# Optimization experiments

Hardware: AMD Instinct MI355X
Metric: run time of the kernel (lower is better)

## Reference

```python
import jax, jax.numpy as jnp
import numpy as np

B = 16384   # tokens
K = 2       # top_k
E = 64      # num_experts
H = 512     # hidden_dim
F = 1024    # expert ffn dim


def setup_inputs() -> dict:
    key = jax.random.key(0)
    k1, k2, k3, k4, k5 = jax.random.split(key, 5)
    hidden_states = jax.random.normal(k1, (B, H), dtype=jnp.float32)
    expert_weights = jax.nn.softmax(jax.random.normal(k2, (B, K), dtype=jnp.float32), axis=-1)
    # Balanced routing: exactly B*K/E assignments per expert (random permutation
    # of a tiled pattern). This is a valid routing for the module and lets the
    # reference use a fixed-capacity grouped GEMM with zero token dropping.
    flat_ids = jax.random.permutation(k3, jnp.tile(jnp.arange(E, dtype=jnp.int32), (B * K) // E))
    expert_ids = flat_ids.reshape(B, K)
    W1 = jax.random.normal(k4, (E, H, F), dtype=jnp.float32) * (1.0 / np.sqrt(H))
    W2 = jax.random.normal(k5, (E, F, H), dtype=jnp.float32) * (1.0 / np.sqrt(F))
    return {"hidden_states": hidden_states, "expert_weights": expert_weights,
            "expert_ids": expert_ids, "W1": W1, "W2": W2}


def reference(hidden_states, expert_weights, expert_ids, W1, W2):
    # Faithful to ExpertGrouping.group_dispatch: every (token, slot) assignment
    # is run through its expert, scaled by its routing weight, and index_add'ed
    # back into the per-token output. Since assignments within an expert are
    # order-independent, we sort assignments by expert id and run one grouped
    # batched GEMM (the fused equivalent of the per-group/per-expert loops).
    b, h = hidden_states.shape
    k = expert_ids.shape[1]
    e = W1.shape[0]
    n = b * k
    cap = n // e  # exact per-expert count (balanced routing)

    flat_ids = expert_ids.reshape(-1)            # [N]
    flat_w = expert_weights.reshape(-1)          # [N]
    token_idx = jnp.arange(n, dtype=jnp.int32) // k  # [N] token for each assignment

    order = jnp.argsort(flat_ids)                # stable sort: groups assignments by expert
    tok_sorted = token_idx[order]                # [N]
    w_sorted = flat_w[order]                     # [N]

    # Gather-dispatch: [E, cap, H]
    xg = hidden_states[tok_sorted].reshape(e, cap, h)
    # Grouped expert FFN (batched over experts)
    hid = jax.nn.silu(jnp.einsum('ech,ehf->ecf', xg, W1))
    yg = jnp.einsum('ecf,efh->ech', hid, W2)     # [E, cap, H]

    # Weighted scatter-combine back to tokens
    weighted = yg.reshape(n, h) * w_sorted[:, None]
    out = jnp.zeros((b, h), dtype=hidden_states.dtype).at[tok_sorted].add(weighted)
    return out
```

## Files before the change

### kernel.cpp

```cpp
#include <hip/hip_runtime.h>
#include <hip/hip_bf16.h>

#define B_TOK 16384
#define TOPK 2
#define NEXP 64
#define HID 512
#define FFN 1024
#define NASSIGN (B_TOK * TOPK)
#define CAP (NASSIGN / NEXP)

typedef unsigned short u16;
typedef __bf16 bf16_t;
typedef bf16_t bf16x8 __attribute__((ext_vector_type(8)));
typedef float f32x4 __attribute__((ext_vector_type(4)));

__device__ __forceinline__ unsigned pkbf(float a, float b) {
  union { bf16_t h[2]; unsigned u; } v;
  v.h[0] = (bf16_t)a; v.h[1] = (bf16_t)b;
  return v.u;
}
__device__ __forceinline__ u16 f2bf(float f) {
  union { bf16_t h; u16 u; } v; v.h = (bf16_t)f; return v.u;
}
__device__ __forceinline__ float bf2f(unsigned u16v) {
  union { unsigned u; float f; } v; v.u = u16v << 16; return v.f;
}

#define GLOAD_LDS16(g, l)                                                     \
  __builtin_amdgcn_global_load_lds((const __attribute__((address_space(1))) void*)(g), \
                                   (__attribute__((address_space(3))) void*)(l), 16, 0, 0)

__global__ void k_route(const int* __restrict__ ids, int* __restrict__ cnt,
                        int* __restrict__ tok_of, int* __restrict__ slot_pos) {
  int n = blockIdx.x * blockDim.x + threadIdx.x;
  if (n >= NASSIGN) return;
  int e = ids[n];
  int r = atomicAdd(&cnt[e], 1);
  int p = e * CAP + r;
  tok_of[p] = n >> 1;
  slot_pos[n] = p;
}

__global__ void k_gather(const float* __restrict__ hs, const int* __restrict__ tok_of,
                         u16* __restrict__ Xg) {
  int p = blockIdx.x * 4 + (threadIdx.x >> 6);
  int lane = threadIdx.x & 63;
  const float4* src = reinterpret_cast<const float4*>(hs + (size_t)tok_of[p] * HID);
  uint2* dst = reinterpret_cast<uint2*>(Xg + (size_t)p * HID);
#pragma unroll
  for (int i = 0; i < 2; i++) {
    float4 v = src[i * 64 + lane];
    uint2 o;
    o.x = pkbf(v.x, v.y);
    o.y = pkbf(v.z, v.w);
    dst[i * 64 + lane] = o;
  }
}

template <int K, int NN, bool SILU>
__global__ __launch_bounds__(256, 2) void k_gemm(const u16* __restrict__ A,
                                                 const float* __restrict__ Wf,
                                                 u16* __restrict__ Cout) {
  constexpr int MT = CAP / 128;
  constexpr int NT = NN / 128;
  constexpr int NWG = NEXP * MT * NT;
  constexpr int Q = NWG / 8;
  constexpr int KT = K / 64;
  int wg = (blockIdx.x % 8) * Q + blockIdx.x / 8;
  int e = wg / (MT * NT);
  int rm = wg % (MT * NT);
  int mt = rm / NT, nt = rm % NT;

  const u16* Ab = A + ((size_t)e * CAP + (size_t)mt * 128) * K;

  __shared__ __align__(16) char smc[65536];

  int t_ = threadIdx.x;
  int lane = t_ & 63, wv = t_ >> 6;
  int wm = wv >> 1, wn = wv & 1;
  int l15 = lane & 15, lhi = lane >> 4;

  int srow = t_ >> 3;
  int gchunk = (t_ & 7) ^ (srow & 7);
  const u16* gA = Ab + (size_t)srow * K + gchunk * 8;
#define STAGE_A(tn)                                                          \
  do {                                                                       \
    char* d_ = smc + ((tn) & 1) * 16384 + wv * 1024;                         \
    const u16* s_ = gA + (size_t)(tn) * 64;                                  \
    GLOAD_LDS16(s_, d_);                                                     \
    GLOAD_LDS16(s_ + (size_t)32 * K, d_ + 4096);                             \
    GLOAD_LDS16(s_ + (size_t)64 * K, d_ + 8192);                             \
    GLOAD_LDS16(s_ + (size_t)96 * K, d_ + 12288);                            \
  } while (0)

  int kunit = t_ >> 5;
  int nunit = t_ & 31;
  const float* gWb = Wf + (size_t)e * K * NN + (size_t)(kunit * 8) * NN +
                     (size_t)nt * 128 + nunit * 4;
  int wbo[4];
#pragma unroll
  for (int i = 0; i < 4; i++) {
    int n = nunit * 4 + i;
    int S = (n ^ (n >> 3)) & 7;
    wbo[i] = 32768 + n * 128 + ((kunit ^ S) << 4);
  }

  f32x4 acc[4][4];
#pragma unroll
  for (int i = 0; i < 4; i++)
#pragma unroll
    for (int j = 0; j < 4; j++) {
      f32x4 z = {0.f, 0.f, 0.f, 0.f};
      acc[i][j] = z;
    }
  bf16x8 a[4][2], b[4][2];

  int aof[4][2], bof[4][2];
#pragma unroll
  for (int f = 0; f < 4; f++) {
    int ar = wm * 64 + f * 16 + l15;
    aof[f][0] = ar * 128 + ((lhi ^ (ar & 7)) << 4);
    aof[f][1] = ar * 128 + (((4 + lhi) ^ (ar & 7)) << 4);
    int br = wn * 64 + f * 16 + l15;
    int Sb = (br ^ (br >> 3)) & 7;
    bof[f][0] = br * 128 + ((lhi ^ Sb) << 4);
    bof[f][1] = br * 128 + (((4 + lhi) ^ Sb) << 4);
  }

#define LOAD_L(tn)                                                           \
  do {                                                                       \
    const float* g_ = gWb + (size_t)(tn) * 64 * NN;                          \
    L0 = *reinterpret_cast<const float4*>(g_);                               \
    L1 = *reinterpret_cast<const float4*>(g_ + (size_t)1 * NN);              \
    L2 = *reinterpret_cast<const float4*>(g_ + (size_t)2 * NN);              \
    L3 = *reinterpret_cast<const float4*>(g_ + (size_t)3 * NN);              \
    L4 = *reinterpret_cast<const float4*>(g_ + (size_t)4 * NN);              \
    L5 = *reinterpret_cast<const float4*>(g_ + (size_t)5 * NN);              \
    L6 = *reinterpret_cast<const float4*>(g_ + (size_t)6 * NN);              \
    L7 = *reinterpret_cast<const float4*>(g_ + (size_t)7 * NN);              \
  } while (0)

#define WRITE_B(bufsel)                                                      \
  do {                                                                       \
    char* w_ = smc + (bufsel) * 16384;                                       \
    _Pragma("unroll") for (int i = 0; i < 4; i++) {                          \
      uint4 v;                                                               \
      v.x = pkbf(L0[i], L1[i]); v.y = pkbf(L2[i], L3[i]);                    \
      v.z = pkbf(L4[i], L5[i]); v.w = pkbf(L6[i], L7[i]);                    \
      *reinterpret_cast<uint4*>(w_ + wbo[i]) = v;                            \
    }                                                                        \
  } while (0)

  float4 L0, L1, L2, L3, L4, L5, L6, L7;

  STAGE_A(0);
  LOAD_L(0);
  asm volatile("s_waitcnt vmcnt(0)" ::: "memory");
  __builtin_amdgcn_sched_barrier(0);
  WRITE_B(0);
  asm volatile("s_waitcnt lgkmcnt(0)" ::: "memory");
  __builtin_amdgcn_sched_barrier(0);
  __builtin_amdgcn_s_barrier();

  for (int t = 0; t < KT; t++) {
    const char* pA = smc + (t & 1) * 16384;
    const char* pB = smc + 32768 + (t & 1) * 16384;
    int nb = (t + 1) & 1;

    if (t + 1 < KT) LOAD_L(t + 1);
#pragma unroll
    for (int f = 0; f < 4; f++) {
      a[f][0] = *reinterpret_cast<const bf16x8*>(pA + aof[f][0]);
      a[f][1] = *reinterpret_cast<const bf16x8*>(pA + aof[f][1]);
      b[f][0] = *reinterpret_cast<const bf16x8*>(pB + bof[f][0]);
      b[f][1] = *reinterpret_cast<const bf16x8*>(pB + bof[f][1]);
    }
    if (t + 1 < KT) STAGE_A(t + 1);
    asm volatile("s_waitcnt lgkmcnt(0)" ::: "memory");
    __builtin_amdgcn_sched_barrier(0);

    __builtin_amdgcn_s_setprio(1);
#pragma unroll
    for (int mf = 0; mf < 4; mf++)
#pragma unroll
      for (int nf = 0; nf < 4; nf++)
#pragma unroll
        for (int kk = 0; kk < 2; kk++)
          acc[mf][nf] = __builtin_amdgcn_mfma_f32_16x16x32_bf16(a[mf][kk], b[nf][kk], acc[mf][nf], 0, 0, 0);
    __builtin_amdgcn_s_setprio(0);

    if (t + 1 < KT) {
      asm volatile("s_waitcnt vmcnt(4)" ::: "memory");
      __builtin_amdgcn_sched_barrier(0);
      WRITE_B(nb);
    }
    asm volatile("s_waitcnt vmcnt(0) lgkmcnt(0)" ::: "memory");
    __builtin_amdgcn_sched_barrier(0);
    __builtin_amdgcn_s_barrier();
  }
#undef STAGE_A
#undef LOAD_L
#undef WRITE_B

#pragma unroll
  for (int mf = 0; mf < 4; mf++) {
#pragma unroll
    for (int nf = 0; nf < 4; nf++) {
#pragma unroll
      for (int rg = 0; rg < 4; rg++) {
        float v = acc[mf][nf][rg];
        int grow = mt * 128 + wm * 64 + mf * 16 + lhi * 4 + rg;
        int gcol = nt * 128 + wn * 64 + nf * 16 + l15;
        size_t off = ((size_t)e * CAP + grow) * NN + gcol;
        if constexpr (SILU) v = v / (1.0f + __expf(-v));
        Cout[off] = f2bf(v);
      }
    }
  }
}

__global__ void k_combine(const u16* __restrict__ yws, const int* __restrict__ slot_pos,
                          const float* __restrict__ w, float* __restrict__ out) {
  int tk = blockIdx.x;
  int t = threadIdx.x;
  int p0 = slot_pos[2 * tk], p1 = slot_pos[2 * tk + 1];
  float w0 = w[2 * tk], w1 = w[2 * tk + 1];
  unsigned ua = reinterpret_cast<const unsigned*>(yws + (size_t)p0 * HID)[t];
  unsigned ub = reinterpret_cast<const unsigned*>(yws + (size_t)p1 * HID)[t];
  float2 o;
  o.x = w0 * bf2f(ua & 0xffffu) + w1 * bf2f(ub & 0xffffu);
  o.y = w0 * bf2f(ua >> 16) + w1 * bf2f(ub >> 16);
  reinterpret_cast<float2*>(out + (size_t)tk * HID)[t] = o;
}

extern "C" void kernel_launch(void* const* d_in, const int* in_sizes, int n_in,
                              void* d_out, int out_size, void* d_ws, size_t ws_size,
                              hipStream_t stream) {
  const float* hs = (const float*)d_in[0];
  const float* wts = (const float*)d_in[1];
  const int* ids = (const int*)d_in[2];
  const float* W1 = (const float*)d_in[3];
  const float* W2 = (const float*)d_in[4];
  float* out = (float*)d_out;

  char* ws = (char*)d_ws;
  size_t o = 0;
  int* cnt = (int*)(ws + o);       o += 1024;
  int* slot_pos = (int*)(ws + o);  o += (size_t)NASSIGN * 4;
  int* tok_of = (int*)(ws + o);    o += (size_t)NASSIGN * 4;
  o = (o + 255) & ~(size_t)255;
  u16* Xg = (u16*)(ws + o);        o += (size_t)NASSIGN * HID * 2;
  u16* hid = (u16*)(ws + o);       o += (size_t)NASSIGN * FFN * 2;
  u16* yws = (u16*)(ws + o);       o += (size_t)NASSIGN * HID * 2;

  hipMemsetAsync(cnt, 0, NEXP * sizeof(int), stream);
  k_route<<<(NASSIGN + 255) / 256, 256, 0, stream>>>(ids, cnt, tok_of, slot_pos);
  k_gather<<<NASSIGN / 4, 256, 0, stream>>>(hs, tok_of, Xg);
  k_gemm<HID, FFN, true><<<NEXP * (CAP / 128) * (FFN / 128), 256, 0, stream>>>(Xg, W1, hid);
  k_gemm<FFN, HID, false><<<NEXP * (CAP / 128) * (HID / 128), 256, 0, stream>>>(hid, W2, yws);
  k_combine<<<B_TOK, 256, 0, stream>>>(yws, slot_pos, wts, out);
}
```

Baseline: 240.5 us.

## Shrink GEMM K-tile to 32 and restructure LDS layout for B operand

Cuts the K step per iteration from 64 to 32, which shrinks LDS use from 64KB to 36KB. The B operand now uses a padded 80-byte row layout instead of an XOR swizzle, loaded as float2 instead of float4. The explicit waitcnt/sched_barrier/setprio scheduling is replaced by plain __syncthreads, and the launch bound min-blocks hint is dropped. The smaller LDS footprint allows more blocks per CU. In exchange there are twice as many iterations and barriers, and less MFMA work between syncs.

```diff
diff --git a/kernel.cpp b/kernel.cpp
--- a/kernel.cpp
+++ b/kernel.cpp
@@ -58,14 +58,14 @@
 }
 
 template <int K, int NN, bool SILU>
-__global__ __launch_bounds__(256, 2) void k_gemm(const u16* __restrict__ A,
-                                                 const float* __restrict__ Wf,
-                                                 u16* __restrict__ Cout) {
+__global__ __launch_bounds__(256) void k_gemm(const u16* __restrict__ A,
+                                              const float* __restrict__ Wf,
+                                              u16* __restrict__ Cout) {
   constexpr int MT = CAP / 128;
   constexpr int NT = NN / 128;
   constexpr int NWG = NEXP * MT * NT;
   constexpr int Q = NWG / 8;
-  constexpr int KT = K / 64;
+  constexpr int KT = K / 32;
   int wg = (blockIdx.x % 8) * Q + blockIdx.x / 8;
   int e = wg / (MT * NT);
   int rm = wg % (MT * NT);
@@ -73,37 +73,52 @@
 
   const u16* Ab = A + ((size_t)e * CAP + (size_t)mt * 128) * K;
 
-  __shared__ __align__(16) char smc[65536];
+  __shared__ __align__(16) char smc[36864];
 
   int t_ = threadIdx.x;
   int lane = t_ & 63, wv = t_ >> 6;
   int wm = wv >> 1, wn = wv & 1;
   int l15 = lane & 15, lhi = lane >> 4;
 
-  int srow = t_ >> 3;
-  int gchunk = (t_ & 7) ^ (srow & 7);
+  int srow = t_ >> 2;
+  int gchunk = (t_ & 3) ^ (srow & 3);
   const u16* gA = Ab + (size_t)srow * K + gchunk * 8;
 #define STAGE_A(tn)                                                          \
   do {                                                                       \
-    char* d_ = smc + ((tn) & 1) * 16384 + wv * 1024;                         \
-    const u16* s_ = gA + (size_t)(tn) * 64;                                  \
+    char* d_ = smc + ((tn) & 1) * 8192 + wv * 1024;                          \
+    const u16* s_ = gA + (size_t)(tn) * 32;                                  \
     GLOAD_LDS16(s_, d_);                                                     \
-    GLOAD_LDS16(s_ + (size_t)32 * K, d_ + 4096);                             \
-    GLOAD_LDS16(s_ + (size_t)64 * K, d_ + 8192);                             \
-    GLOAD_LDS16(s_ + (size_t)96 * K, d_ + 12288);                            \
+    GLOAD_LDS16(s_ + (size_t)64 * K, d_ + 4096);                             \
   } while (0)
 
-  int kunit = t_ >> 5;
-  int nunit = t_ & 31;
-  const float* gWb = Wf + (size_t)e * K * NN + (size_t)(kunit * 8) * NN +
-                     (size_t)nt * 128 + nunit * 4;
-  int wbo[4];
-#pragma unroll
-  for (int i = 0; i < 4; i++) {
-    int n = nunit * 4 + i;
-    int S = (n ^ (n >> 3)) & 7;
-    wbo[i] = 32768 + n * 128 + ((kunit ^ S) << 4);
-  }
+  int kg = t_ >> 6;
+  int ng = t_ & 63;
+  const float* gWb = Wf + (size_t)e * K * NN + (size_t)(kg * 8) * NN +
+                     (size_t)nt * 128 + ng * 2;
+  float2 L0, L1, L2, L3, L4, L5, L6, L7;
+#define LOAD_L(tn)                                                           \
+  do {                                                                       \
+    const float* g_ = gWb + (size_t)(tn) * 32 * NN;                          \
+    L0 = *reinterpret_cast<const float2*>(g_);                               \
+    L1 = *reinterpret_cast<const float2*>(g_ + (size_t)1 * NN);              \
+    L2 = *reinterpret_cast<const float2*>(g_ + (size_t)2 * NN);              \
+    L3 = *reinterpret_cast<const float2*>(g_ + (size_t)3 * NN);              \
+    L4 = *reinterpret_cast<const float2*>(g_ + (size_t)4 * NN);              \
+    L5 = *reinterpret_cast<const float2*>(g_ + (size_t)5 * NN);              \
+    L6 = *reinterpret_cast<const float2*>(g_ + (size_t)6 * NN);              \
+    L7 = *reinterpret_cast<const float2*>(g_ + (size_t)7 * NN);              \
+  } while (0)
+#define WRITE_B(tn)                                                          \
+  do {                                                                       \
+    char* w_ = smc + 16384 + ((tn) & 1) * 10240 + kg * 16;                   \
+    uint4 v0, v1;                                                            \
+    v0.x = pkbf(L0.x, L1.x); v0.y = pkbf(L2.x, L3.x);                        \
+    v0.z = pkbf(L4.x, L5.x); v0.w = pkbf(L6.x, L7.x);                        \
+    v1.x = pkbf(L0.y, L1.y); v1.y = pkbf(L2.y, L3.y);                        \
+    v1.z = pkbf(L4.y, L5.y); v1.w = pkbf(L6.y, L7.y);                        \
+    *reinterpret_cast<uint4*>(w_ + (ng * 2) * 80) = v0;                      \
+    *reinterpret_cast<uint4*>(w_ + (ng * 2 + 1) * 80) = v1;                  \
+  } while (0)
 
   f32x4 acc[4][4];
 #pragma unroll
@@ -113,90 +128,42 @@
       f32x4 z = {0.f, 0.f, 0.f, 0.f};
       acc[i][j] = z;
     }
-  bf16x8 a[4][2], b[4][2];
-
-  int aof[4][2], bof[4][2];
+  bf16x8 a[4], b[4];
+
+  int aof[4], bof[4];
 #pragma unroll
   for (int f = 0; f < 4; f++) {
     int ar = wm * 64 + f * 16 + l15;
-    aof[f][0] = ar * 128 + ((lhi ^ (ar & 7)) << 4);
-    aof[f][1] = ar * 128 + (((4 + lhi) ^ (ar & 7)) << 4);
+    aof[f] = ar * 64 + ((lhi ^ (ar & 3)) << 4);
     int br = wn * 64 + f * 16 + l15;
-    int Sb = (br ^ (br >> 3)) & 7;
-    bof[f][0] = br * 128 + ((lhi ^ Sb) << 4);
-    bof[f][1] = br * 128 + (((4 + lhi) ^ Sb) << 4);
-  }
-
-#define LOAD_L(tn)                                                           \
-  do {                                                                       \
-    const float* g_ = gWb + (size_t)(tn) * 64 * NN;                          \
-    L0 = *reinterpret_cast<const float4*>(g_);                               \
-    L1 = *reinterpret_cast<const float4*>(g_ + (size_t)1 * NN);              \
-    L2 = *reinterpret_cast<const float4*>(g_ + (size_t)2 * NN);              \
-    L3 = *reinterpret_cast<const float4*>(g_ + (size_t)3 * NN);              \
-    L4 = *reinterpret_cast<const float4*>(g_ + (size_t)4 * NN);              \
-    L5 = *reinterpret_cast<const float4*>(g_ + (size_t)5 * NN);              \
-    L6 = *reinterpret_cast<const float4*>(g_ + (size_t)6 * NN);              \
-    L7 = *reinterpret_cast<const float4*>(g_ + (size_t)7 * NN);              \
-  } while (0)
-
-#define WRITE_B(bufsel)                                                      \
-  do {                                                                       \
-    char* w_ = smc + (bufsel) * 16384;                                       \
-    _Pragma("unroll") for (int i = 0; i < 4; i++) {                          \
-      uint4 v;                                                               \
-      v.x = pkbf(L0[i], L1[i]); v.y = pkbf(L2[i], L3[i]);                    \
-      v.z = pkbf(L4[i], L5[i]); v.w = pkbf(L6[i], L7[i]);                    \
-      *reinterpret_cast<uint4*>(w_ + wbo[i]) = v;                            \
-    }                                                                        \
-  } while (0)
-
-  float4 L0, L1, L2, L3, L4, L5, L6, L7;
+    bof[f] = br * 80 + (lhi << 4);
+  }
 
   STAGE_A(0);
   LOAD_L(0);
-  asm volatile("s_waitcnt vmcnt(0)" ::: "memory");
-  __builtin_amdgcn_sched_barrier(0);
   WRITE_B(0);
-  asm volatile("s_waitcnt lgkmcnt(0)" ::: "memory");
-  __builtin_amdgcn_sched_barrier(0);
-  __builtin_amdgcn_s_barrier();
+  __syncthreads();
 
   for (int t = 0; t < KT; t++) {
-    const char* pA = smc + (t & 1) * 16384;
-    const char* pB = smc + 32768 + (t & 1) * 16384;
-    int nb = (t + 1) & 1;
+    const char* pA = smc + (t & 1) * 8192;
+    const char* pB = smc + 16384 + (t & 1) * 10240;
 
     if (t + 1 < KT) LOAD_L(t + 1);
 #pragma unroll
     for (int f = 0; f < 4; f++) {
-      a[f][0] = *reinterpret_cast<const bf16x8*>(pA + aof[f][0]);
-      a[f][1] = *reinterpret_cast<const bf16x8*>(pA + aof[f][1]);
-      b[f][0] = *reinterpret_cast<const bf16x8*>(pB + bof[f][0]);
-      b[f][1] = *reinterpret_cast<const bf16x8*>(pB + bof[f][1]);
+      a[f] = *reinterpret_cast<const bf16x8*>(pA + aof[f]);
+      b[f] = *reinterpret_cast<const bf16x8*>(pB + bof[f]);
     }
     if (t + 1 < KT) STAGE_A(t + 1);
-    asm volatile("s_waitcnt lgkmcnt(0)" ::: "memory");
-    __builtin_amdgcn_sched_barrier(0);
-
-    __builtin_amdgcn_s_setprio(1);
+
 #pragma unroll
     for (int mf = 0; mf < 4; mf++)
 #pragma unroll
       for (int nf = 0; nf < 4; nf++)
-#pragma unroll
-        for (int kk = 0; kk < 2; kk++)
-          acc[mf][nf] = __builtin_amdgcn_mfma_f32_16x16x32_bf16(a[mf][kk], b[nf][kk], acc[mf][nf], 0, 0, 0);
-    __builtin_amdgcn_s_setprio(0);
-
-    if (t + 1 < KT) {
-      asm volatile("s_waitcnt vmcnt(4)" ::: "memory");
-      __builtin_amdgcn_sched_barrier(0);
-      WRITE_B(nb);
-    }
-    asm volatile("s_waitcnt vmcnt(0) lgkmcnt(0)" ::: "memory");
-    __builtin_amdgcn_sched_barrier(0);
-    __builtin_amdgcn_s_barrier();
+        acc[mf][nf] = __builtin_amdgcn_mfma_f32_16x16x32_bf16(a[mf], b[nf], acc[mf][nf], 0, 0, 0);
+
+    if (t + 1 < KT) WRITE_B(t + 1);
+    __syncthreads();
   }
 #undef STAGE_A
 #undef LOAD_L
```

After: 271.7 us. 13.0% more time.
